# Performance work log

Hardware: AMD Instinct MI355X
Metric: run time of the kernel (lower is better)

The kernel has to match this reference:

```python
import jax, jax.numpy as jnp
import numpy as np

EMBED_DIM = 1024
NUM_HEADS = 16
HEAD_DIM = EMBED_DIM // NUM_HEADS
B, T = 4, 2048


def setup_inputs() -> dict:
    key = jax.random.key(0)
    ks = jax.random.split(key, 5)
    s = 1.0 / np.sqrt(EMBED_DIM)
    x = jax.random.normal(ks[0], (B, T, EMBED_DIM), dtype=jnp.float32)
    W_qkv = jax.random.uniform(ks[1], (EMBED_DIM, 3 * EMBED_DIM), minval=-s, maxval=s, dtype=jnp.float32)
    b_qkv = jax.random.uniform(ks[2], (3 * EMBED_DIM,), minval=-s, maxval=s, dtype=jnp.float32)
    W_proj = jax.random.uniform(ks[3], (EMBED_DIM, EMBED_DIM), minval=-s, maxval=s, dtype=jnp.float32)
    b_proj = jax.random.uniform(ks[4], (EMBED_DIM,), minval=-s, maxval=s, dtype=jnp.float32)
    return {"x": x, "W_qkv": W_qkv, "b_qkv": b_qkv, "W_proj": W_proj, "b_proj": b_proj}


def reference(x, W_qkv, b_qkv, W_proj, b_proj):
    Bq, Tq, C = x.shape
    H, D = NUM_HEADS, HEAD_DIM
    qkv = x @ W_qkv + b_qkv                      # [B,T,3C]
    qkv = qkv.reshape(Bq, Tq, 3, H, D)
    q = qkv[:, :, 0].transpose(0, 2, 1, 3)       # [B,H,T,D]
    k = qkv[:, :, 1].transpose(0, 2, 1, 3)
    v = qkv[:, :, 2].transpose(0, 2, 1, 3)
    scale = 1.0 / jnp.sqrt(jnp.asarray(D, x.dtype))
    attn = jnp.einsum('bhqd,bhkd->bhqk', q, k) * scale  # [B,H,T,T]
    mask = jnp.tril(jnp.ones((Tq, Tq), dtype=bool))     # causal: keep lower triangle
    attn = jnp.where(mask, attn, jnp.asarray(-jnp.inf, attn.dtype))
    attn = jax.nn.softmax(attn, axis=-1)
    out = jnp.einsum('bhqk,bhkd->bhqd', attn, v)        # [B,H,T,D]
    out = out.transpose(0, 2, 1, 3).reshape(Bq, Tq, C)
    return out @ W_proj + b_proj
```

## Files before the change

kernel.cpp:

```cpp
#include <hip/hip_runtime.h>
#include <stdint.h>

typedef unsigned short ushort_t;
typedef __attribute__((ext_vector_type(4))) unsigned int  u32x4;
typedef __attribute__((ext_vector_type(2))) unsigned int  u32x2;
typedef __attribute__((ext_vector_type(4))) float         f32x4;
typedef __attribute__((ext_vector_type(8))) __bf16        bf16x8;
typedef __attribute__((ext_vector_type(2))) __bf16        bf16x2;

__device__ __forceinline__ ushort_t f2bf(float f) {
    unsigned int u = __float_as_uint(f);
    u += 0x7fffu + ((u >> 16) & 1u);
    return (ushort_t)(u >> 16);
}
__device__ __forceinline__ unsigned int pack2bf(float a, float b) {
    return (unsigned int)f2bf(a) | ((unsigned int)f2bf(b) << 16);
}
#if __has_builtin(__builtin_amdgcn_cvt_pk_bf16_f32)
__device__ __forceinline__ unsigned int pack2bf_fast(float a, float b) {
    bf16x2 v = __builtin_amdgcn_cvt_pk_bf16_f32(a, b);
    return __builtin_bit_cast(unsigned int, v);
}
#else
__device__ __forceinline__ unsigned int pack2bf_fast(float a, float b) {
    return pack2bf(a, b);
}
#endif
__device__ __forceinline__ f32x4 mfma16(bf16x8 a, bf16x8 b, f32x4 c) {
    return __builtin_amdgcn_mfma_f32_16x16x32_bf16(a, b, c, 0, 0, 0);
}
__device__ __forceinline__ bf16x8 ldfrag(const ushort_t* p) {
    return __builtin_bit_cast(bf16x8, *(const u32x4*)p);
}

__device__ __forceinline__ void gld16(const ushort_t* g, ushort_t* l) {
    __builtin_amdgcn_global_load_lds(
        (const __attribute__((address_space(1))) void*)g,
        (__attribute__((address_space(3))) void*)l, 16, 0, 0);
}

__device__ __forceinline__ void wg_barrier() {
    asm volatile("s_waitcnt lgkmcnt(0)\n\ts_barrier" ::: "memory");
}

#define QSCALE 0.18033688011112042f

__global__ __launch_bounds__(256) void prep(const float* __restrict__ X,
                                            ushort_t* __restrict__ Xb,
                                            const float* __restrict__ Wq,
                                            ushort_t* __restrict__ Wqt,
                                            const float* __restrict__ Wp,
                                            ushort_t* __restrict__ Wpt) {
    __shared__ float tile[32][33];
    const int tid = threadIdx.x;
    const int b   = blockIdx.x;
    if (b < 4096) {
        long i = ((long)b * 256 + tid) * 8;
        float4 a = *(const float4*)(X + i);
        float4 c = *(const float4*)(X + i + 4);
        u32x4 pk;
        pk.x = pack2bf(a.x, a.y); pk.y = pack2bf(a.z, a.w);
        pk.z = pack2bf(c.x, c.y); pk.w = pack2bf(c.z, c.w);
        *(u32x4*)(Xb + i) = pk;
        return;
    }
    const float* W; ushort_t* Wt; int N, bx, by;
    if (b < 7168) { int idx = b - 4096; W = Wq; Wt = Wqt; N = 3072; bx = idx % 96; by = idx / 96; }
    else          { int idx = b - 7168; W = Wp; Wt = Wpt; N = 1024; bx = idx & 31; by = idx >> 5; }
    const int tx = tid & 31, ty = tid >> 5;
    const int n0 = bx * 32, k0 = by * 32;
    for (int p = 0; p < 4; ++p)
        tile[ty + 8*p][tx] = W[(long)(k0 + ty + 8*p) * N + n0 + tx];
    __syncthreads();
    for (int p = 0; p < 4; ++p)
        Wt[(long)(n0 + ty + 8*p) * 1024 + k0 + tx] = f2bf(tile[tx][ty + 8*p]);
}

__global__ __launch_bounds__(256) void gemm_qkv(const ushort_t* __restrict__ Xb,
                                                const ushort_t* __restrict__ Wt,
                                                const float* __restrict__ bias,
                                                ushort_t* __restrict__ Qo,
                                                ushort_t* __restrict__ Ko,
                                                ushort_t* __restrict__ Vto) {
    __shared__ __align__(16) ushort_t smem[24576];

    const int tid  = threadIdx.x;
    const int g    = blockIdx.x;
    const int grp  = g / 192, rr = g % 192;
    const int m0   = (grp * 8 + (rr & 7)) * 128;
    const int n0   = (rr >> 3) * 128;
    const int lane = tid & 63, w = tid >> 6;
    const int quad = lane >> 4, l16 = lane & 15;
    const int wm = (w >> 1) * 64, wn = (w & 1) * 64;

    const int srow  = tid >> 2;
    const int slot  = tid & 3;
    const int oct   = slot ^ ((tid >> 3) & 3);
    const int rslot = (quad ^ ((l16 >> 1) & 3)) * 8;
    const int wbase = (tid & 192) * 8;

    const ushort_t* Ap = Xb + (long)(m0 + srow) * 1024 + oct * 8;
    const ushort_t* Bp = Wt + (long)(n0 + srow) * 1024 + oct * 8;

    f32x4 acc[4][4] = {};

    auto issue = [&](int pf, int ibuf) {
        int k = (pf < 32) ? (pf << 5) : 0;
        gld16(Ap + k,         &smem[ibuf + wbase]);
        gld16(Ap + k + 65536, &smem[ibuf + wbase + 2048]);
        gld16(Bp + k,         &smem[ibuf + wbase + 4096]);
        gld16(Bp + k + 65536, &smem[ibuf + wbase + 6144]);
    };
    auto step = [&](int p, int rbuf, int ibuf) {
        asm volatile("s_waitcnt vmcnt(4)\n\ts_barrier" ::: "memory");
        issue(p + 2, ibuf);
        const ushort_t* As = smem + rbuf;
        const ushort_t* Bs = As + 4096;
        bf16x8 af[4], bfr[4];
        for (int i = 0; i < 4; ++i)
            af[i] = ldfrag(&As[(wm + 16*i + l16) * 32 + rslot]);
        for (int j = 0; j < 4; ++j)
            bfr[j] = ldfrag(&Bs[(wn + 16*j + l16) * 32 + rslot]);
        __builtin_amdgcn_s_setprio(1);
        for (int i = 0; i < 4; ++i)
            for (int j = 0; j < 4; ++j)
                acc[i][j] = mfma16(af[i], bfr[j], acc[i][j]);
        __builtin_amdgcn_s_setprio(0);
    };

    issue(0, 0);
    issue(1, 8192);
    for (int p = 0; p < 30; p += 3) {
        step(p,     0,     16384);
        step(p + 1, 8192,  0);
        step(p + 2, 16384, 8192);
    }
    step(30, 0,    16384);
    step(31, 8192, 0);

    float bj[4];
    for (int j = 0; j < 4; ++j) bj[j] = bias[n0 + wn + 16*j + l16];
    const int bb = m0 >> 11, t0m = m0 & 2047;
    asm volatile("s_waitcnt vmcnt(0)" ::: "memory");
    __syncthreads();

    if (n0 < 2048) {
        ushort_t* dst = (n0 < 1024) ? Qo : Ko;
        const float scale = (n0 < 1024) ? QSCALE : 1.0f;
        const int nbase = (n0 < 1024) ? n0 : n0 - 1024;
        for (int i = 0; i < 4; ++i)
            for (int j = 0; j < 4; ++j) {
                int nl = wn + 16*j + l16;
                for (int r = 0; r < 4; ++r) {
                    int ml = wm + 16*i + quad*4 + r;
                    smem[ml * 136 + nl] = f2bf((acc[i][j][r] + bj[j]) * scale);
                }
            }
        __syncthreads();
        for (int c = 0; c < 8; ++c) {
            int chunk = tid + 256 * c;
            int row = chunk >> 4, nc = (chunk & 15) * 8;
            int n = nbase + nc;
            int hh = n >> 6, d = n & 63;
            *(u32x4*)&dst[((long)(bb*16 + hh) * 2048 + t0m + row) * 64 + d] =
                *(const u32x4*)&smem[row * 136 + nc];
        }
    } else {
        for (int i = 0; i < 4; ++i)
            for (int j = 0; j < 4; ++j) {
                int nl = wn + 16*j + l16;
                for (int r = 0; r < 4; ++r) {
                    int ml = wm + 16*i + quad*4 + r;
                    smem[nl * 136 + ml] = f2bf(acc[i][j][r] + bj[j]);
                }
            }
        __syncthreads();
        for (int c = 0; c < 8; ++c) {
            int chunk = tid + 256 * c;
            int row = chunk >> 4, mc = (chunk & 15) * 8;
            int n = n0 - 2048 + row;
            int hh = n >> 6, d = n & 63;
            *(u32x4*)&Vto[((long)(bb*16 + hh) * 64 + d) * 2048 + t0m + mc] =
                *(const u32x4*)&smem[row * 136 + mc];
        }
    }
}

__global__ __launch_bounds__(256) void attn_kernel(const ushort_t* __restrict__ Q,
                                                   const ushort_t* __restrict__ K,
                                                   const ushort_t* __restrict__ Vt,
                                                   ushort_t* __restrict__ O) {
    __shared__ __align__(16) ushort_t Ks[2][64 * 64];
    __shared__ __align__(16) ushort_t Vs[2][64 * 64];
    __shared__ __align__(16) ushort_t Ps[128 * 72];

    const int tid  = threadIdx.x;
    const int lane = tid & 63, w = tid >> 6, quad = lane >> 4, l16 = lane & 15;
    const int g    = blockIdx.x;
    const int bh   = (g & 7) + 8 * ((g >> 3) & 7);
    const int qt   = 15 - (g >> 6);
    const ushort_t* qptr = Q  + (long)bh * 2048 * 64;
    const ushort_t* kptr = K  + (long)bh * 2048 * 64;
    const ushort_t* vptr = Vt + (long)bh * 64 * 2048;
    const int bb2 = bh >> 4, h = bh & 15;

    const int srow = tid >> 3;
    const int slot = tid & 7;
    const int oct  = slot ^ (srow & 7);
    const int koff = srow * 64 + oct * 8;
    const int voff = srow * 2048 + oct * 8;
    const int wofs = srow * 64 + slot * 8;

    const int qbase = qt * 128;
    const int nkt = 2 * qt + 2;

    for (int c = 0; c < 4; ++c) {
        int flat = tid + 256 * c;
        int row = flat >> 3, kc = (flat & 7) * 8;
        *(u32x4*)&Ps[row * 72 + kc] = *(const u32x4*)&qptr[(long)(qbase + row) * 64 + kc];
    }
    wg_barrier();
    bf16x8 qf[2][2];
    for (int nt = 0; nt < 2; ++nt)
        for (int kk = 0; kk < 2; ++kk)
            qf[nt][kk] = ldfrag(&Ps[(32*w + 16*nt + l16) * 72 + kk*32 + quad*8]);

    f32x4 acc[2][4] = {};
    float l_run[2] = {0.f, 0.f};

    auto phase = [&](int kt, ushort_t* Kb, ushort_t* Vb) {
        const int kbase = kt * 64;
        if (kbase > qbase + 32*w + 31) return;
        f32x4 s[4][2] = {};
        __builtin_amdgcn_s_setprio(1);
        for (int kk = 0; kk < 2; ++kk)
            for (int mt = 0; mt < 4; ++mt) {
                bf16x8 kf = ldfrag(&Kb[(16*mt + l16) * 64 + ((4*kk + quad) ^ (l16 & 7)) * 8]);
                for (int nt = 0; nt < 2; ++nt)
                    s[mt][nt] = mfma16(kf, qf[nt][kk], s[mt][nt]);
            }
        __builtin_amdgcn_s_setprio(0);
        if (kbase + 63 > qbase + 32*w) {
            for (int mt = 0; mt < 4; ++mt)
                for (int nt = 0; nt < 2; ++nt) {
                    int qv = qbase + 32*w + 16*nt + l16;
                    for (int r = 0; r < 4; ++r)
                        if (kbase + 16*mt + 4*quad + r > qv)
                            s[mt][nt][r] = -__builtin_inff();
                }
        }
        for (int nt = 0; nt < 2; ++nt)
            for (int mt = 0; mt < 4; ++mt) {
                float p0 = __builtin_amdgcn_exp2f(s[mt][nt][0]);
                float p1 = __builtin_amdgcn_exp2f(s[mt][nt][1]);
                float p2 = __builtin_amdgcn_exp2f(s[mt][nt][2]);
                float p3 = __builtin_amdgcn_exp2f(s[mt][nt][3]);
                l_run[nt] += (p0 + p1) + (p2 + p3);
                u32x2 pk;
                pk.x = pack2bf_fast(p0, p1);
                pk.y = pack2bf_fast(p2, p3);
                *(u32x2*)&Ps[(32*w + 16*nt + l16) * 72 + 16*mt + 4*quad] = pk;
            }
        __builtin_amdgcn_s_setprio(1);
        for (int kk = 0; kk < 2; ++kk) {
            bf16x8 pf0 = ldfrag(&Ps[(32*w + l16) * 72 + kk*32 + quad*8]);
            bf16x8 pf1 = ldfrag(&Ps[(32*w + 16 + l16) * 72 + kk*32 + quad*8]);
            for (int jd = 0; jd < 4; ++jd) {
                bf16x8 vf = ldfrag(&Vb[(16*jd + l16) * 64 + ((4*kk + quad) ^ (l16 & 7)) * 8]);
                acc[0][jd] = mfma16(pf0, vf, acc[0][jd]);
                acc[1][jd] = mfma16(pf1, vf, acc[1][jd]);
            }
        }
        __builtin_amdgcn_s_setprio(0);
    };

    u32x4 KA0 = *(const u32x4*)(kptr + koff);
    u32x4 KA1 = *(const u32x4*)(kptr + koff + 2048);
    u32x4 VA0 = *(const u32x4*)(vptr + voff);
    u32x4 VA1 = *(const u32x4*)(vptr + voff + 65536);
    u32x4 KB0 = *(const u32x4*)(kptr + 4096 + koff);
    u32x4 KB1 = *(const u32x4*)(kptr + 4096 + koff + 2048);
    u32x4 VB0 = *(const u32x4*)(vptr + 64 + voff);
    u32x4 VB1 = *(const u32x4*)(vptr + 64 + voff + 65536);

    for (int kt = 0; kt < nkt; kt += 2) {
        {
            *(u32x4*)&Ks[0][wofs]        = KA0;
            *(u32x4*)&Ks[0][wofs + 2048] = KA1;
            *(u32x4*)&Vs[0][wofs]        = VA0;
            *(u32x4*)&Vs[0][wofs + 2048] = VA1;
            int kf = (kt + 2 < nkt) ? kt + 2 : kt;
            KA0 = *(const u32x4*)(kptr + kf*4096 + koff);
            KA1 = *(const u32x4*)(kptr + kf*4096 + koff + 2048);
            VA0 = *(const u32x4*)(vptr + kf*64 + voff);
            VA1 = *(const u32x4*)(vptr + kf*64 + voff + 65536);
            wg_barrier();
            phase(kt, Ks[0], Vs[0]);
        }
        {
            *(u32x4*)&Ks[1][wofs]        = KB0;
            *(u32x4*)&Ks[1][wofs + 2048] = KB1;
            *(u32x4*)&Vs[1][wofs]        = VB0;
            *(u32x4*)&Vs[1][wofs + 2048] = VB1;
            int kf = (kt + 3 < nkt) ? kt + 3 : kt + 1;
            KB0 = *(const u32x4*)(kptr + kf*4096 + koff);
            KB1 = *(const u32x4*)(kptr + kf*4096 + koff + 2048);
            VB0 = *(const u32x4*)(vptr + kf*64 + voff);
            VB1 = *(const u32x4*)(vptr + kf*64 + voff + 65536);
            wg_barrier();
            phase(kt + 1, Ks[1], Vs[1]);
        }
    }

    for (int i = 0; i < 2; ++i) {
        float l = l_run[i];
        l += __shfl_xor(l, 16, 64);
        l += __shfl_xor(l, 32, 64);
        for (int r = 0; r < 4; ++r) {
            float linv = 1.0f / __shfl(l, (lane & 48) | (4*quad + r), 64);
            int t = qbase + 32*w + 16*i + 4*quad + r;
            for (int jd = 0; jd < 4; ++jd) {
                int d = 16*jd + l16;
                O[((long)(bb2*2048 + t)) * 1024 + h*64 + d] = f2bf(acc[i][jd][r] * linv);
            }
        }
    }
}

__global__ __launch_bounds__(256) void gemm_proj(const ushort_t* __restrict__ A,
                                                 const ushort_t* __restrict__ Wt,
                                                 const float* __restrict__ bias,
                                                 float* __restrict__ Out) {
    __shared__ __align__(16) ushort_t smem[24576];

    const int tid  = threadIdx.x;
    const int g    = blockIdx.x;
    const int grp  = g / 64, rr = g % 64;
    const int m0   = (grp * 8 + (rr & 7)) * 128;
    const int n0   = (rr >> 3) * 128;
    const int lane = tid & 63, w = tid >> 6;
    const int quad = lane >> 4, l16 = lane & 15;
    const int wm = (w >> 1) * 64, wn = (w & 1) * 64;

    const int srow  = tid >> 2;
    const int slot  = tid & 3;
    const int oct   = slot ^ ((tid >> 3) & 3);
    const int rslot = (quad ^ ((l16 >> 1) & 3)) * 8;
    const int wbase = (tid & 192) * 8;

    const ushort_t* Ap = A  + (long)(m0 + srow) * 1024 + oct * 8;
    const ushort_t* Bp = Wt + (long)(n0 + srow) * 1024 + oct * 8;

    f32x4 acc[4][4] = {};

    auto issue = [&](int pf, int ibuf) {
        int k = (pf < 32) ? (pf << 5) : 0;
        gld16(Ap + k,         &smem[ibuf + wbase]);
        gld16(Ap + k + 65536, &smem[ibuf + wbase + 2048]);
        gld16(Bp + k,         &smem[ibuf + wbase + 4096]);
        gld16(Bp + k + 65536, &smem[ibuf + wbase + 6144]);
    };
    auto step = [&](int p, int rbuf, int ibuf) {
        asm volatile("s_waitcnt vmcnt(4)\n\ts_barrier" ::: "memory");
        issue(p + 2, ibuf);
        const ushort_t* As = smem + rbuf;
        const ushort_t* Bs = As + 4096;
        bf16x8 af[4], bfr[4];
        for (int i = 0; i < 4; ++i)
            af[i] = ldfrag(&As[(wm + 16*i + l16) * 32 + rslot]);
        for (int j = 0; j < 4; ++j)
            bfr[j] = ldfrag(&Bs[(wn + 16*j + l16) * 32 + rslot]);
        __builtin_amdgcn_s_setprio(1);
        for (int i = 0; i < 4; ++i)
            for (int j = 0; j < 4; ++j)
                acc[i][j] = mfma16(af[i], bfr[j], acc[i][j]);
        __builtin_amdgcn_s_setprio(0);
    };

    issue(0, 0);
    issue(1, 8192);
    for (int p = 0; p < 30; p += 3) {
        step(p,     0,     16384);
        step(p + 1, 8192,  0);
        step(p + 2, 16384, 8192);
    }
    step(30, 0,    16384);
    step(31, 8192, 0);
    asm volatile("s_waitcnt vmcnt(0)" ::: "memory");

    float bj[4];
    for (int j = 0; j < 4; ++j) bj[j] = bias[n0 + wn + 16*j + l16];
    for (int i = 0; i < 4; ++i)
        for (int j = 0; j < 4; ++j)
            for (int r = 0; r < 4; ++r) {
                int m = m0 + wm + 16*i + quad*4 + r;
                int n = n0 + wn + 16*j + l16;
                Out[(long)m * 1024 + n] = acc[i][j][r] + bj[j];
            }
}

extern "C" void kernel_launch(void* const* d_in, const int* in_sizes, int n_in,
                              void* d_out, int out_size, void* d_ws, size_t ws_size,
                              hipStream_t stream) {
    const float* x     = (const float*)d_in[0];
    const float* Wqkv  = (const float*)d_in[1];
    const float* bqkv  = (const float*)d_in[2];
    const float* Wproj = (const float*)d_in[3];
    const float* bproj = (const float*)d_in[4];
    float* out = (float*)d_out;

    ushort_t* wqkvt  = (ushort_t*)d_ws;
    ushort_t* wprojt = wqkvt  + 3072 * 1024;
    ushort_t* Qb     = wprojt + 1024 * 1024;
    ushort_t* Kb     = Qb  + 8388608;
    ushort_t* Vtb    = Kb  + 8388608;
    ushort_t* XbA2   = Vtb + 8388608;

    prep<<<8192, 256, 0, stream>>>(x, XbA2, Wqkv, wqkvt, Wproj, wprojt);
    gemm_qkv<<<1536, 256, 0, stream>>>(XbA2, wqkvt, bqkv, Qb, Kb, Vtb);
    attn_kernel<<<1024, 256, 0, stream>>>(Qb, Kb, Vtb, XbA2);
    gemm_proj<<<512, 256, 0, stream>>>(XbA2, wprojt, bproj, out);
}
```

Before: 242.4 us.

## Load GEMM A fragments directly from global into registers, keep only B in LDS

Both the QKV and projection GEMMs stop staging the activation (A) tile through shared memory. Each wave now loads its own A MFMA fragments straight from global memory into registers, one k-step ahead. Only the weight tile still uses the global-to-LDS triple buffer, which shrinks LDS use and raises the launch-bounds occupancy hint to 3 blocks. The cost is redundant global A loads, since waves sharing rows each fetch them, plus more exposed global-load latency because the register prefetch is only one step deep.

```diff
diff --git a/kernel.cpp b/kernel.cpp
--- a/kernel.cpp
+++ b/kernel.cpp
@@ -31,6 +31,9 @@
 }
 __device__ __forceinline__ bf16x8 ldfrag(const ushort_t* p) {
     return __builtin_bit_cast(bf16x8, *(const u32x4*)p);
+}
+__device__ __forceinline__ bf16x8 asfrag(u32x4 v) {
+    return __builtin_bit_cast(bf16x8, v);
 }
 
 __device__ __forceinline__ void gld16(const ushort_t* g, ushort_t* l) {
@@ -76,13 +79,13 @@
         Wt[(long)(n0 + ty + 8*p) * 1024 + k0 + tx] = f2bf(tile[tx][ty + 8*p]);
 }
 
-__global__ __launch_bounds__(256) void gemm_qkv(const ushort_t* __restrict__ Xb,
-                                                const ushort_t* __restrict__ Wt,
-                                                const float* __restrict__ bias,
-                                                ushort_t* __restrict__ Qo,
-                                                ushort_t* __restrict__ Ko,
-                                                ushort_t* __restrict__ Vto) {
-    __shared__ __align__(16) ushort_t smem[24576];
+__global__ __launch_bounds__(256, 3) void gemm_qkv(const ushort_t* __restrict__ Xb,
+                                                   const ushort_t* __restrict__ Wt,
+                                                   const float* __restrict__ bias,
+                                                   ushort_t* __restrict__ Qo,
+                                                   ushort_t* __restrict__ Ko,
+                                                   ushort_t* __restrict__ Vto) {
+    __shared__ __align__(16) ushort_t smem[17408];
 
     const int tid  = threadIdx.x;
     const int g    = blockIdx.x;
@@ -99,44 +102,45 @@
     const int rslot = (quad ^ ((l16 >> 1) & 3)) * 8;
     const int wbase = (tid & 192) * 8;
 
-    const ushort_t* Ap = Xb + (long)(m0 + srow) * 1024 + oct * 8;
     const ushort_t* Bp = Wt + (long)(n0 + srow) * 1024 + oct * 8;
+    const ushort_t* A0 = Xb + (long)(m0 + wm + l16) * 1024 + quad * 8;
 
     f32x4 acc[4][4] = {};
-
-    auto issue = [&](int pf, int ibuf) {
+    u32x4 acur[4];
+
+    auto issueB = [&](int pf, int ibuf) {
         int k = (pf < 32) ? (pf << 5) : 0;
-        gld16(Ap + k,         &smem[ibuf + wbase]);
-        gld16(Ap + k + 65536, &smem[ibuf + wbase + 2048]);
-        gld16(Bp + k,         &smem[ibuf + wbase + 4096]);
-        gld16(Bp + k + 65536, &smem[ibuf + wbase + 6144]);
+        gld16(Bp + k,         &smem[ibuf + wbase]);
+        gld16(Bp + k + 65536, &smem[ibuf + wbase + 2048]);
     };
     auto step = [&](int p, int rbuf, int ibuf) {
-        asm volatile("s_waitcnt vmcnt(4)\n\ts_barrier" ::: "memory");
-        issue(p + 2, ibuf);
-        const ushort_t* As = smem + rbuf;
-        const ushort_t* Bs = As + 4096;
-        bf16x8 af[4], bfr[4];
-        for (int i = 0; i < 4; ++i)
-            af[i] = ldfrag(&As[(wm + 16*i + l16) * 32 + rslot]);
+        asm volatile("s_waitcnt vmcnt(6)\n\ts_barrier" ::: "memory");
+        issueB(p + 2, ibuf);
+        const ushort_t* Bs = smem + rbuf;
+        bf16x8 bfr[4];
         for (int j = 0; j < 4; ++j)
             bfr[j] = ldfrag(&Bs[(wn + 16*j + l16) * 32 + rslot]);
         __builtin_amdgcn_s_setprio(1);
         for (int i = 0; i < 4; ++i)
             for (int j = 0; j < 4; ++j)
-                acc[i][j] = mfma16(af[i], bfr[j], acc[i][j]);
+                acc[i][j] = mfma16(asfrag(acur[i]), bfr[j], acc[i][j]);
         __builtin_amdgcn_s_setprio(0);
+        int kn = (p + 1 < 32) ? ((p + 1) << 5) : 0;
+        for (int i = 0; i < 4; ++i)
+            acur[i] = *(const u32x4*)(A0 + i * 16384 + kn);
     };
 
-    issue(0, 0);
-    issue(1, 8192);
+    issueB(0, 0);
+    issueB(1, 4096);
+    for (int i = 0; i < 4; ++i)
+        acur[i] = *(const u32x4*)(A0 + i * 16384);
     for (int p = 0; p < 30; p += 3) {
-        step(p,     0,     16384);
-        step(p + 1, 8192,  0);
-        step(p + 2, 16384, 8192);
-    }
-    step(30, 0,    16384);
-    step(31, 8192, 0);
+        step(p,     0,    8192);
+        step(p + 1, 4096, 0);
+        step(p + 2, 8192, 4096);
+    }
+    step(30, 0,    8192);
+    step(31, 4096, 0);
 
     float bj[4];
     for (int j = 0; j < 4; ++j) bj[j] = bias[n0 + wn + 16*j + l16];
@@ -327,11 +331,11 @@
     }
 }
 
-__global__ __launch_bounds__(256) void gemm_proj(const ushort_t* __restrict__ A,
-                                                 const ushort_t* __restrict__ Wt,
-                                                 const float* __restrict__ bias,
-                                                 float* __restrict__ Out) {
-    __shared__ __align__(16) ushort_t smem[24576];
+__global__ __launch_bounds__(256, 3) void gemm_proj(const ushort_t* __restrict__ A,
+                                                    const ushort_t* __restrict__ Wt,
+                                                    const float* __restrict__ bias,
+                                                    float* __restrict__ Out) {
+    __shared__ __align__(16) ushort_t smem[12288];
 
     const int tid  = threadIdx.x;
     const int g    = blockIdx.x;
@@ -348,44 +352,45 @@
     const int rslot = (quad ^ ((l16 >> 1) & 3)) * 8;
     const int wbase = (tid & 192) * 8;
 
-    const ushort_t* Ap = A  + (long)(m0 + srow) * 1024 + oct * 8;
     const ushort_t* Bp = Wt + (long)(n0 + srow) * 1024 + oct * 8;
+    const ushort_t* A0 = A + (long)(m0 + wm + l16) * 1024 + quad * 8;
 
     f32x4 acc[4][4] = {};
-
-    auto issue = [&](int pf, int ibuf) {
+    u32x4 acur[4];
+
+    auto issueB = [&](int pf, int ibuf) {
         int k = (pf < 32) ? (pf << 5) : 0;
-        gld16(Ap + k,         &smem[ibuf + wbase]);
-        gld16(Ap + k + 65536, &smem[ibuf + wbase + 2048]);
-        gld16(Bp + k,         &smem[ibuf + wbase + 4096]);
-        gld16(Bp + k + 65536, &smem[ibuf + wbase + 6144]);
+        gld16(Bp + k,         &smem[ibuf + wbase]);
+        gld16(Bp + k + 65536, &smem[ibuf + wbase + 2048]);
     };
     auto step = [&](int p, int rbuf, int ibuf) {
-        asm volatile("s_waitcnt vmcnt(4)\n\ts_barrier" ::: "memory");
-        issue(p + 2, ibuf);
-        const ushort_t* As = smem + rbuf;
-        const ushort_t* Bs = As + 4096;
-        bf16x8 af[4], bfr[4];
-        for (int i = 0; i < 4; ++i)
-            af[i] = ldfrag(&As[(wm + 16*i + l16) * 32 + rslot]);
+        asm volatile("s_waitcnt vmcnt(6)\n\ts_barrier" ::: "memory");
+        issueB(p + 2, ibuf);
+        const ushort_t* Bs = smem + rbuf;
+        bf16x8 bfr[4];
         for (int j = 0; j < 4; ++j)
             bfr[j] = ldfrag(&Bs[(wn + 16*j + l16) * 32 + rslot]);
         __builtin_amdgcn_s_setprio(1);
         for (int i = 0; i < 4; ++i)
             for (int j = 0; j < 4; ++j)
-                acc[i][j] = mfma16(af[i], bfr[j], acc[i][j]);
+                acc[i][j] = mfma16(asfrag(acur[i]), bfr[j], acc[i][j]);
         __builtin_amdgcn_s_setprio(0);
+        int kn = (p + 1 < 32) ? ((p + 1) << 5) : 0;
+        for (int i = 0; i < 4; ++i)
+            acur[i] = *(const u32x4*)(A0 + i * 16384 + kn);
     };
 
-    issue(0, 0);
-    issue(1, 8192);
+    issueB(0, 0);
+    issueB(1, 4096);
+    for (int i = 0; i < 4; ++i)
+        acur[i] = *(const u32x4*)(A0 + i * 16384);
     for (int p = 0; p < 30; p += 3) {
-        step(p,     0,     16384);
-        step(p + 1, 8192,  0);
-        step(p + 2, 16384, 8192);
-    }
-    step(30, 0,    16384);
-    step(31, 8192, 0);
+        step(p,     0,    8192);
+        step(p + 1, 4096, 0);
+        step(p + 2, 8192, 4096);
+    }
+    step(30, 0,    8192);
+    step(31, 4096, 0);
     asm volatile("s_waitcnt vmcnt(0)" ::: "memory");
 
     float bj[4];
```

After: 302.6 us. +24.9%, slower.

## Enlarge QKV GEMM tiles to 256x256 with 512-thread blocks

Applied to the files above, without the earlier changes.

The QKV projection GEMM moves from 128x128 tiles with 256 threads to 256x256 tiles with 512 threads (8 waves, each computing 128x64). It uses a double-buffered pipeline with split MFMA phases and a new XCD-aware block swizzle. The epilogue is staged through LDS in four passes to fit the larger tile. The aim is more operand reuse per global load and fewer blocks, at the cost of extra barriers and register pressure. With 384 blocks the grid may not fill all CUs evenly.

```diff
diff --git a/kernel.cpp b/kernel.cpp
--- a/kernel.cpp
+++ b/kernel.cpp
@@ -76,17 +76,288 @@
         Wt[(long)(n0 + ty + 8*p) * 1024 + k0 + tx] = f2bf(tile[tx][ty + 8*p]);
 }
 
-__global__ __launch_bounds__(256) void gemm_qkv(const ushort_t* __restrict__ Xb,
-                                                const ushort_t* __restrict__ Wt,
-                                                const float* __restrict__ bias,
-                                                ushort_t* __restrict__ Qo,
-                                                ushort_t* __restrict__ Ko,
-                                                ushort_t* __restrict__ Vto) {
-    __shared__ __align__(16) ushort_t smem[24576];
+__global__ __launch_bounds__(512, 4) void gemm_qkv(const ushort_t* __restrict__ Xb,
+                                                   const ushort_t* __restrict__ Wt,
+                                                   const float* __restrict__ bias,
+                                                   ushort_t* __restrict__ Qo,
+                                                   ushort_t* __restrict__ Ko,
+                                                   ushort_t* __restrict__ Vto) {
+    __shared__ __align__(16) ushort_t smem[32768];
 
     const int tid  = threadIdx.x;
     const int g    = blockIdx.x;
-    const int grp  = g / 192, rr = g % 192;
+    const int swz  = (g & 7) * 48 + (g >> 3);
+    const int m0   = (swz & 31) * 256;
+    const int n0   = (swz >> 5) * 256;
+    const int lane = tid & 63, w = tid >> 6;
+    const int quad = lane >> 4, l16 = lane & 15;
+    const int wm   = (w >> 2) * 128, wn = (w & 3) * 64;
+
+    const int srow  = tid >> 2;
+    const int slot  = tid & 3;
+    const int oct   = slot ^ ((tid >> 3) & 3);
+    const int rslot = (quad ^ ((l16 >> 1) & 3)) * 8;
+
+    const ushort_t* ApL = Xb + (long)(m0 + srow) * 1024 + oct * 8;
+    const ushort_t* ApH = ApL + 131072;
+    const ushort_t* BpL = Wt + (long)(n0 + srow) * 1024 + oct * 8;
+    const ushort_t* BpH = BpL + 131072;
+
+    f32x4 acc[8][4] = {};
+
+    auto issue_tile = [&](int kt, int bbase) {
+        int k = (kt < 32) ? (kt << 5) : 0;
+        gld16(ApL + k, &smem[bbase + tid * 8]);
+        gld16(ApH + k, &smem[bbase + 4096 + tid * 8]);
+        gld16(BpL + k, &smem[bbase + 8192 + tid * 8]);
+        gld16(BpH + k, &smem[bbase + 12288 + tid * 8]);
+    };
+
+    auto tile_step = [&](int t, int rb, int ib) {
+        const ushort_t* As = smem + rb;
+        const ushort_t* Bs = smem + rb + 8192;
+        bf16x8 af[4], bfj[4];
+        for (int i = 0; i < 4; ++i)
+            af[i] = ldfrag(&As[(wm + 16*i + l16) * 32 + rslot]);
+        for (int j = 0; j < 4; ++j)
+            bfj[j] = ldfrag(&Bs[(wn + 16*j + l16) * 32 + rslot]);
+        issue_tile(t + 1, ib);
+        asm volatile("s_barrier" ::: "memory");
+        __builtin_amdgcn_sched_barrier(0);
+        __builtin_amdgcn_s_setprio(1);
+        for (int i = 0; i < 4; ++i)
+            for (int j = 0; j < 4; ++j)
+                acc[i][j] = mfma16(af[i], bfj[j], acc[i][j]);
+        __builtin_amdgcn_s_setprio(0);
+        asm volatile("s_barrier" ::: "memory");
+        bf16x8 ag[4];
+        for (int i = 0; i < 4; ++i)
+            ag[i] = ldfrag(&As[(wm + 64 + 16*i + l16) * 32 + rslot]);
+        asm volatile("s_barrier" ::: "memory");
+        __builtin_amdgcn_sched_barrier(0);
+        __builtin_amdgcn_s_setprio(1);
+        for (int i = 0; i < 4; ++i)
+            for (int j = 0; j < 4; ++j)
+                acc[4 + i][j] = mfma16(ag[i], bfj[j], acc[4 + i][j]);
+        __builtin_amdgcn_s_setprio(0);
+        asm volatile("s_waitcnt vmcnt(0)\n\ts_barrier" ::: "memory");
+    };
+
+    issue_tile(0, 0);
+    asm volatile("s_waitcnt vmcnt(0)\n\ts_barrier" ::: "memory");
+    for (int t = 0; t < 32; t += 2) {
+        tile_step(t,     0,     16384);
+        tile_step(t + 1, 16384, 0);
+    }
+
+    float bj[4];
+    for (int j = 0; j < 4; ++j) bj[j] = bias[n0 + wn + 16*j + l16];
+    const int bb = m0 >> 11, t0m = m0 & 2047;
+    __syncthreads();
+
+    if (n0 < 2048) {
+        ushort_t* dst = (n0 < 1024) ? Qo : Ko;
+        const float scale = (n0 < 1024) ? QSCALE : 1.0f;
+        const int nbase = (n0 < 1024) ? n0 : n0 - 1024;
+        for (int p = 0; p < 4; ++p) {
+            if (wm == (p >> 1) * 128) {
+                int i0 = (p & 1) * 4;
+                for (int ii = 0; ii < 4; ++ii)
+                    for (int j = 0; j < 4; ++j) {
+                        int nl = wn + 16*j + l16;
+                        for (int r = 0; r < 4; ++r) {
+                            int lr = 16*ii + quad*4 + r;
+                            smem[lr * 264 + nl] = f2bf((acc[i0 + ii][j][r] + bj[j]) * scale);
+                        }
+                    }
+            }
+            __syncthreads();
+            for (int c = 0; c < 4; ++c) {
+                int chunk = tid + 512 * c;
+                int row = chunk >> 5, nc = (chunk & 31) * 8;
+                int n = nbase + nc;
+                int hh = n >> 6, d = n & 63;
+                *(u32x4*)&dst[((long)(bb*16 + hh) * 2048 + t0m + 64*p + row) * 64 + d] =
+                    *(const u32x4*)&smem[row * 264 + nc];
+            }
+            __syncthreads();
+        }
+    } else {
+        for (int p = 0; p < 4; ++p) {
+            if (wn == 64 * p) {
+                for (int i = 0; i < 8; ++i)
+                    for (int j = 0; j < 4; ++j) {
+                        int nl = 16*j + l16;
+                        for (int r = 0; r < 4; ++r) {
+                            int ml = wm + 16*i + quad*4 + r;
+                            smem[nl * 264 + ml] = f2bf(acc[i][j][r] + bj[j]);
+                        }
+                    }
+            }
+            __syncthreads();
+            for (int c = 0; c < 4; ++c) {
+                int chunk = tid + 512 * c;
+                int nr = chunk >> 5, mc = (chunk & 31) * 8;
+                int n = n0 - 2048 + 64*p + nr;
+                int hh = n >> 6, d = n & 63;
+                *(u32x4*)&Vto[((long)(bb*16 + hh) * 64 + d) * 2048 + t0m + mc] =
+                    *(const u32x4*)&smem[nr * 264 + mc];
+            }
+            __syncthreads();
+        }
+    }
+}
+
+__global__ __launch_bounds__(256) void attn_kernel(const ushort_t* __restrict__ Q,
+                                                   const ushort_t* __restrict__ K,
+                                                   const ushort_t* __restrict__ Vt,
+                                                   ushort_t* __restrict__ O) {
+    __shared__ __align__(16) ushort_t Ks[2][64 * 64];
+    __shared__ __align__(16) ushort_t Vs[2][64 * 64];
+    __shared__ __align__(16) ushort_t Ps[128 * 72];
+
+    const int tid  = threadIdx.x;
+    const int lane = tid & 63, w = tid >> 6, quad = lane >> 4, l16 = lane & 15;
+    const int g    = blockIdx.x;
+    const int bh   = (g & 7) + 8 * ((g >> 3) & 7);
+    const int qt   = 15 - (g >> 6);
+    const ushort_t* qptr = Q  + (long)bh * 2048 * 64;
+    const ushort_t* kptr = K  + (long)bh * 2048 * 64;
+    const ushort_t* vptr = Vt + (long)bh * 64 * 2048;
+    const int bb2 = bh >> 4, h = bh & 15;
+
+    const int srow = tid >> 3;
+    const int slot = tid & 7;
+    const int oct  = slot ^ (srow & 7);
+    const int koff = srow * 64 + oct * 8;
+    const int voff = srow * 2048 + oct * 8;
+    const int wofs = srow * 64 + slot * 8;
+
+    const int qbase = qt * 128;
+    const int nkt = 2 * qt + 2;
+
+    for (int c = 0; c < 4; ++c) {
+        int flat = tid + 256 * c;
+        int row = flat >> 3, kc = (flat & 7) * 8;
+        *(u32x4*)&Ps[row * 72 + kc] = *(const u32x4*)&qptr[(long)(qbase + row) * 64 + kc];
+    }
+    wg_barrier();
+    bf16x8 qf[2][2];
+    for (int nt = 0; nt < 2; ++nt)
+        for (int kk = 0; kk < 2; ++kk)
+            qf[nt][kk] = ldfrag(&Ps[(32*w + 16*nt + l16) * 72 + kk*32 + quad*8]);
+
+    f32x4 acc[2][4] = {};
+    float l_run[2] = {0.f, 0.f};
+
+    auto phase = [&](int kt, ushort_t* Kb, ushort_t* Vb) {
+        const int kbase = kt * 64;
+        if (kbase > qbase + 32*w + 31) return;
+        f32x4 s[4][2] = {};
+        __builtin_amdgcn_s_setprio(1);
+        for (int kk = 0; kk < 2; ++kk)
+            for (int mt = 0; mt < 4; ++mt) {
+                bf16x8 kf = ldfrag(&Kb[(16*mt + l16) * 64 + ((4*kk + quad) ^ (l16 & 7)) * 8]);
+                for (int nt = 0; nt < 2; ++nt)
+                    s[mt][nt] = mfma16(kf, qf[nt][kk], s[mt][nt]);
+            }
+        __builtin_amdgcn_s_setprio(0);
+        if (kbase + 63 > qbase + 32*w) {
+            for (int mt = 0; mt < 4; ++mt)
+                for (int nt = 0; nt < 2; ++nt) {
+                    int qv = qbase + 32*w + 16*nt + l16;
+                    for (int r = 0; r < 4; ++r)
+                        if (kbase + 16*mt + 4*quad + r > qv)
+                            s[mt][nt][r] = -__builtin_inff();
+                }
+        }
+        for (int nt = 0; nt < 2; ++nt)
+            for (int mt = 0; mt < 4; ++mt) {
+                float p0 = __builtin_amdgcn_exp2f(s[mt][nt][0]);
+                float p1 = __builtin_amdgcn_exp2f(s[mt][nt][1]);
+                float p2 = __builtin_amdgcn_exp2f(s[mt][nt][2]);
+                float p3 = __builtin_amdgcn_exp2f(s[mt][nt][3]);
+                l_run[nt] += (p0 + p1) + (p2 + p3);
+                u32x2 pk;
+                pk.x = pack2bf_fast(p0, p1);
+                pk.y = pack2bf_fast(p2, p3);
+                *(u32x2*)&Ps[(32*w + 16*nt + l16) * 72 + 16*mt + 4*quad] = pk;
+            }
+        __builtin_amdgcn_s_setprio(1);
+        for (int kk = 0; kk < 2; ++kk) {
+            bf16x8 pf0 = ldfrag(&Ps[(32*w + l16) * 72 + kk*32 + quad*8]);
+            bf16x8 pf1 = ldfrag(&Ps[(32*w + 16 + l16) * 72 + kk*32 + quad*8]);
+            for (int jd = 0; jd < 4; ++jd) {
+                bf16x8 vf = ldfrag(&Vb[(16*jd + l16) * 64 + ((4*kk + quad) ^ (l16 & 7)) * 8]);
+                acc[0][jd] = mfma16(pf0, vf, acc[0][jd]);
+                acc[1][jd] = mfma16(pf1, vf, acc[1][jd]);
+            }
+        }
+        __builtin_amdgcn_s_setprio(0);
+    };
+
+    u32x4 KA0 = *(const u32x4*)(kptr + koff);
+    u32x4 KA1 = *(const u32x4*)(kptr + koff + 2048);
+    u32x4 VA0 = *(const u32x4*)(vptr + voff);
+    u32x4 VA1 = *(const u32x4*)(vptr + voff + 65536);
+    u32x4 KB0 = *(const u32x4*)(kptr + 4096 + koff);
+    u32x4 KB1 = *(const u32x4*)(kptr + 4096 + koff + 2048);
+    u32x4 VB0 = *(const u32x4*)(vptr + 64 + voff);
+    u32x4 VB1 = *(const u32x4*)(vptr + 64 + voff + 65536);
+
+    for (int kt = 0; kt < nkt; kt += 2) {
+        {
+            *(u32x4*)&Ks[0][wofs]        = KA0;
+            *(u32x4*)&Ks[0][wofs + 2048] = KA1;
+            *(u32x4*)&Vs[0][wofs]        = VA0;
+            *(u32x4*)&Vs[0][wofs + 2048] = VA1;
+            int kf = (kt + 2 < nkt) ? kt + 2 : kt;
+            KA0 = *(const u32x4*)(kptr + kf*4096 + koff);
+            KA1 = *(const u32x4*)(kptr + kf*4096 + koff + 2048);
+            VA0 = *(const u32x4*)(vptr + kf*64 + voff);
+            VA1 = *(const u32x4*)(vptr + kf*64 + voff + 65536);
+            wg_barrier();
+            phase(kt, Ks[0], Vs[0]);
+        }
+        {
+            *(u32x4*)&Ks[1][wofs]        = KB0;
+            *(u32x4*)&Ks[1][wofs + 2048] = KB1;
+            *(u32x4*)&Vs[1][wofs]        = VB0;
+            *(u32x4*)&Vs[1][wofs + 2048] = VB1;
+            int kf = (kt + 3 < nkt) ? kt + 3 : kt + 1;
+            KB0 = *(const u32x4*)(kptr + kf*4096 + koff);
+            KB1 = *(const u32x4*)(kptr + kf*4096 + koff + 2048);
+            VB0 = *(const u32x4*)(vptr + kf*64 + voff);
+            VB1 = *(const u32x4*)(vptr + kf*64 + voff + 65536);
+            wg_barrier();
+            phase(kt + 1, Ks[1], Vs[1]);
+        }
+    }
+
+    for (int i = 0; i < 2; ++i) {
+        float l = l_run[i];
+        l += __shfl_xor(l, 16, 64);
+        l += __shfl_xor(l, 32, 64);
+        for (int r = 0; r < 4; ++r) {
+            float linv = 1.0f / __shfl(l, (lane & 48) | (4*quad + r), 64);
+            int t = qbase + 32*w + 16*i + 4*quad + r;
+            for (int jd = 0; jd < 4; ++jd) {
+                int d = 16*jd + l16;
+                O[((long)(bb2*2048 + t)) * 1024 + h*64 + d] = f2bf(acc[i][jd][r] * linv);
+            }
+        }
+    }
+}
+
+__global__ __launch_bounds__(256) void gemm_proj(const ushort_t* __restrict__ A,
+                                                 const ushort_t* __restrict__ Wt,
+                                                 const float* __restrict__ bias,
+                                                 float* __restrict__ Out) {
+    __shared__ __align__(16) ushort_t smem[24576];
+
+    const int tid  = threadIdx.x;
+    const int g    = blockIdx.x;
+    const int grp  = g / 64, rr = g % 64;
     const int m0   = (grp * 8 + (rr & 7)) * 128;
     const int n0   = (rr >> 3) * 128;
     const int lane = tid & 63, w = tid >> 6;
@@ -99,7 +370,7 @@
     const int rslot = (quad ^ ((l16 >> 1) & 3)) * 8;
     const int wbase = (tid & 192) * 8;
 
-    const ushort_t* Ap = Xb + (long)(m0 + srow) * 1024 + oct * 8;
+    const ushort_t* Ap = A  + (long)(m0 + srow) * 1024 + oct * 8;
     const ushort_t* Bp = Wt + (long)(n0 + srow) * 1024 + oct * 8;
 
     f32x4 acc[4][4] = {};
@@ -137,255 +408,6 @@
     }
     step(30, 0,    16384);
     step(31, 8192, 0);
-
-    float bj[4];
-    for (int j = 0; j < 4; ++j) bj[j] = bias[n0 + wn + 16*j + l16];
-    const int bb = m0 >> 11, t0m = m0 & 2047;
-    asm volatile("s_waitcnt vmcnt(0)" ::: "memory");
-    __syncthreads();
-
-    if (n0 < 2048) {
-        ushort_t* dst = (n0 < 1024) ? Qo : Ko;
-        const float scale = (n0 < 1024) ? QSCALE : 1.0f;
-        const int nbase = (n0 < 1024) ? n0 : n0 - 1024;
-        for (int i = 0; i < 4; ++i)
-            for (int j = 0; j < 4; ++j) {
-                int nl = wn + 16*j + l16;
-                for (int r = 0; r < 4; ++r) {
-                    int ml = wm + 16*i + quad*4 + r;
-                    smem[ml * 136 + nl] = f2bf((acc[i][j][r] + bj[j]) * scale);
-                }
-            }
-        __syncthreads();
-        for (int c = 0; c < 8; ++c) {
-            int chunk = tid + 256 * c;
-            int row = chunk >> 4, nc = (chunk & 15) * 8;
-            int n = nbase + nc;
-            int hh = n >> 6, d = n & 63;
-            *(u32x4*)&dst[((long)(bb*16 + hh) * 2048 + t0m + row) * 64 + d] =
-                *(const u32x4*)&smem[row * 136 + nc];
-        }
-    } else {
-        for (int i = 0; i < 4; ++i)
-            for (int j = 0; j < 4; ++j) {
-                int nl = wn + 16*j + l16;
-                for (int r = 0; r < 4; ++r) {
-                    int ml = wm + 16*i + quad*4 + r;
-                    smem[nl * 136 + ml] = f2bf(acc[i][j][r] + bj[j]);
-                }
-            }
-        __syncthreads();
-        for (int c = 0; c < 8; ++c) {
-            int chunk = tid + 256 * c;
-            int row = chunk >> 4, mc = (chunk & 15) * 8;
-            int n = n0 - 2048 + row;
-            int hh = n >> 6, d = n & 63;
-            *(u32x4*)&Vto[((long)(bb*16 + hh) * 64 + d) * 2048 + t0m + mc] =
-                *(const u32x4*)&smem[row * 136 + mc];
-        }
-    }
-}
-
-__global__ __launch_bounds__(256) void attn_kernel(const ushort_t* __restrict__ Q,
-                                                   const ushort_t* __restrict__ K,
-                                                   const ushort_t* __restrict__ Vt,
-                                                   ushort_t* __restrict__ O) {
-    __shared__ __align__(16) ushort_t Ks[2][64 * 64];
-    __shared__ __align__(16) ushort_t Vs[2][64 * 64];
-    __shared__ __align__(16) ushort_t Ps[128 * 72];
-
-    const int tid  = threadIdx.x;
-    const int lane = tid & 63, w = tid >> 6, quad = lane >> 4, l16 = lane & 15;
-    const int g    = blockIdx.x;
-    const int bh   = (g & 7) + 8 * ((g >> 3) & 7);
-    const int qt   = 15 - (g >> 6);
-    const ushort_t* qptr = Q  + (long)bh * 2048 * 64;
-    const ushort_t* kptr = K  + (long)bh * 2048 * 64;
-    const ushort_t* vptr = Vt + (long)bh * 64 * 2048;
-    const int bb2 = bh >> 4, h = bh & 15;
-
-    const int srow = tid >> 3;
-    const int slot = tid & 7;
-    const int oct  = slot ^ (srow & 7);
-    const int koff = srow * 64 + oct * 8;
-    const int voff = srow * 2048 + oct * 8;
-    const int wofs = srow * 64 + slot * 8;
-
-    const int qbase = qt * 128;
-    const int nkt = 2 * qt + 2;
-
-    for (int c = 0; c < 4; ++c) {
-        int flat = tid + 256 * c;
-        int row = flat >> 3, kc = (flat & 7) * 8;
-        *(u32x4*)&Ps[row * 72 + kc] = *(const u32x4*)&qptr[(long)(qbase + row) * 64 + kc];
-    }
-    wg_barrier();
-    bf16x8 qf[2][2];
-    for (int nt = 0; nt < 2; ++nt)
-        for (int kk = 0; kk < 2; ++kk)
-            qf[nt][kk] = ldfrag(&Ps[(32*w + 16*nt + l16) * 72 + kk*32 + quad*8]);
-
-    f32x4 acc[2][4] = {};
-    float l_run[2] = {0.f, 0.f};
-
-    auto phase = [&](int kt, ushort_t* Kb, ushort_t* Vb) {
-        const int kbase = kt * 64;
-        if (kbase > qbase + 32*w + 31) return;
-        f32x4 s[4][2] = {};
-        __builtin_amdgcn_s_setprio(1);
-        for (int kk = 0; kk < 2; ++kk)
-            for (int mt = 0; mt < 4; ++mt) {
-                bf16x8 kf = ldfrag(&Kb[(16*mt + l16) * 64 + ((4*kk + quad) ^ (l16 & 7)) * 8]);
-                for (int nt = 0; nt < 2; ++nt)
-                    s[mt][nt] = mfma16(kf, qf[nt][kk], s[mt][nt]);
-            }
-        __builtin_amdgcn_s_setprio(0);
-        if (kbase + 63 > qbase + 32*w) {
-            for (int mt = 0; mt < 4; ++mt)
-                for (int nt = 0; nt < 2; ++nt) {
-                    int qv = qbase + 32*w + 16*nt + l16;
-                    for (int r = 0; r < 4; ++r)
-                        if (kbase + 16*mt + 4*quad + r > qv)
-                            s[mt][nt][r] = -__builtin_inff();
-                }
-        }
-        for (int nt = 0; nt < 2; ++nt)
-            for (int mt = 0; mt < 4; ++mt) {
-                float p0 = __builtin_amdgcn_exp2f(s[mt][nt][0]);
-                float p1 = __builtin_amdgcn_exp2f(s[mt][nt][1]);
-                float p2 = __builtin_amdgcn_exp2f(s[mt][nt][2]);
-                float p3 = __builtin_amdgcn_exp2f(s[mt][nt][3]);
-                l_run[nt] += (p0 + p1) + (p2 + p3);
-                u32x2 pk;
-                pk.x = pack2bf_fast(p0, p1);
-                pk.y = pack2bf_fast(p2, p3);
-                *(u32x2*)&Ps[(32*w + 16*nt + l16) * 72 + 16*mt + 4*quad] = pk;
-            }
-        __builtin_amdgcn_s_setprio(1);
-        for (int kk = 0; kk < 2; ++kk) {
-            bf16x8 pf0 = ldfrag(&Ps[(32*w + l16) * 72 + kk*32 + quad*8]);
-            bf16x8 pf1 = ldfrag(&Ps[(32*w + 16 + l16) * 72 + kk*32 + quad*8]);
-            for (int jd = 0; jd < 4; ++jd) {
-                bf16x8 vf = ldfrag(&Vb[(16*jd + l16) * 64 + ((4*kk + quad) ^ (l16 & 7)) * 8]);
-                acc[0][jd] = mfma16(pf0, vf, acc[0][jd]);
-                acc[1][jd] = mfma16(pf1, vf, acc[1][jd]);
-            }
-        }
-        __builtin_amdgcn_s_setprio(0);
-    };
-
-    u32x4 KA0 = *(const u32x4*)(kptr + koff);
-    u32x4 KA1 = *(const u32x4*)(kptr + koff + 2048);
-    u32x4 VA0 = *(const u32x4*)(vptr + voff);
-    u32x4 VA1 = *(const u32x4*)(vptr + voff + 65536);
-    u32x4 KB0 = *(const u32x4*)(kptr + 4096 + koff);
-    u32x4 KB1 = *(const u32x4*)(kptr + 4096 + koff + 2048);
-    u32x4 VB0 = *(const u32x4*)(vptr + 64 + voff);
-    u32x4 VB1 = *(const u32x4*)(vptr + 64 + voff + 65536);
-
-    for (int kt = 0; kt < nkt; kt += 2) {
-        {
-            *(u32x4*)&Ks[0][wofs]        = KA0;
-            *(u32x4*)&Ks[0][wofs + 2048] = KA1;
-            *(u32x4*)&Vs[0][wofs]        = VA0;
-            *(u32x4*)&Vs[0][wofs + 2048] = VA1;
-            int kf = (kt + 2 < nkt) ? kt + 2 : kt;
-            KA0 = *(const u32x4*)(kptr + kf*4096 + koff);
-            KA1 = *(const u32x4*)(kptr + kf*4096 + koff + 2048);
-            VA0 = *(const u32x4*)(vptr + kf*64 + voff);
-            VA1 = *(const u32x4*)(vptr + kf*64 + voff + 65536);
-            wg_barrier();
-            phase(kt, Ks[0], Vs[0]);
-        }
-        {
-            *(u32x4*)&Ks[1][wofs]        = KB0;
-            *(u32x4*)&Ks[1][wofs + 2048] = KB1;
-            *(u32x4*)&Vs[1][wofs]        = VB0;
-            *(u32x4*)&Vs[1][wofs + 2048] = VB1;
-            int kf = (kt + 3 < nkt) ? kt + 3 : kt + 1;
-            KB0 = *(const u32x4*)(kptr + kf*4096 + koff);
-            KB1 = *(const u32x4*)(kptr + kf*4096 + koff + 2048);
-            VB0 = *(const u32x4*)(vptr + kf*64 + voff);
-            VB1 = *(const u32x4*)(vptr + kf*64 + voff + 65536);
-            wg_barrier();
-            phase(kt + 1, Ks[1], Vs[1]);
-        }
-    }
-
-    for (int i = 0; i < 2; ++i) {
-        float l = l_run[i];
-        l += __shfl_xor(l, 16, 64);
-        l += __shfl_xor(l, 32, 64);
-        for (int r = 0; r < 4; ++r) {
-            float linv = 1.0f / __shfl(l, (lane & 48) | (4*quad + r), 64);
-            int t = qbase + 32*w + 16*i + 4*quad + r;
-            for (int jd = 0; jd < 4; ++jd) {
-                int d = 16*jd + l16;
-                O[((long)(bb2*2048 + t)) * 1024 + h*64 + d] = f2bf(acc[i][jd][r] * linv);
-            }
-        }
-    }
-}
-
-__global__ __launch_bounds__(256) void gemm_proj(const ushort_t* __restrict__ A,
-                                                 const ushort_t* __restrict__ Wt,
-                                                 const float* __restrict__ bias,
-                                                 float* __restrict__ Out) {
-    __shared__ __align__(16) ushort_t smem[24576];
-
-    const int tid  = threadIdx.x;
-    const int g    = blockIdx.x;
-    const int grp  = g / 64, rr = g % 64;
-    const int m0   = (grp * 8 + (rr & 7)) * 128;
-    const int n0   = (rr >> 3) * 128;
-    const int lane = tid & 63, w = tid >> 6;
-    const int quad = lane >> 4, l16 = lane & 15;
-    const int wm = (w >> 1) * 64, wn = (w & 1) * 64;
-
-    const int srow  = tid >> 2;
-    const int slot  = tid & 3;
-    const int oct   = slot ^ ((tid >> 3) & 3);
-    const int rslot = (quad ^ ((l16 >> 1) & 3)) * 8;
-    const int wbase = (tid & 192) * 8;
-
-    const ushort_t* Ap = A  + (long)(m0 + srow) * 1024 + oct * 8;
-    const ushort_t* Bp = Wt + (long)(n0 + srow) * 1024 + oct * 8;
-
-    f32x4 acc[4][4] = {};
-
-    auto issue = [&](int pf, int ibuf) {
-        int k = (pf < 32) ? (pf << 5) : 0;
-        gld16(Ap + k,         &smem[ibuf + wbase]);
-        gld16(Ap + k + 65536, &smem[ibuf + wbase + 2048]);
-        gld16(Bp + k,         &smem[ibuf + wbase + 4096]);
-        gld16(Bp + k + 65536, &smem[ibuf + wbase + 6144]);
-    };
-    auto step = [&](int p, int rbuf, int ibuf) {
-        asm volatile("s_waitcnt vmcnt(4)\n\ts_barrier" ::: "memory");
-        issue(p + 2, ibuf);
-        const ushort_t* As = smem + rbuf;
-        const ushort_t* Bs = As + 4096;
-        bf16x8 af[4], bfr[4];
-        for (int i = 0; i < 4; ++i)
-            af[i] = ldfrag(&As[(wm + 16*i + l16) * 32 + rslot]);
-        for (int j = 0; j < 4; ++j)
-            bfr[j] = ldfrag(&Bs[(wn + 16*j + l16) * 32 + rslot]);
-        __builtin_amdgcn_s_setprio(1);
-        for (int i = 0; i < 4; ++i)
-            for (int j = 0; j < 4; ++j)
-                acc[i][j] = mfma16(af[i], bfr[j], acc[i][j]);
-        __builtin_amdgcn_s_setprio(0);
-    };
-
-    issue(0, 0);
-    issue(1, 8192);
-    for (int p = 0; p < 30; p += 3) {
-        step(p,     0,     16384);
-        step(p + 1, 8192,  0);
-        step(p + 2, 16384, 8192);
-    }
-    step(30, 0,    16384);
-    step(31, 8192, 0);
     asm volatile("s_waitcnt vmcnt(0)" ::: "memory");
 
     float bj[4];
@@ -417,7 +439,7 @@
     ushort_t* XbA2   = Vtb + 8388608;
 
     prep<<<8192, 256, 0, stream>>>(x, XbA2, Wqkv, wqkvt, Wproj, wprojt);
-    gemm_qkv<<<1536, 256, 0, stream>>>(XbA2, wqkvt, bqkv, Qb, Kb, Vtb);
+    gemm_qkv<<<384, 512, 0, stream>>>(XbA2, wqkvt, bqkv, Qb, Kb, Vtb);
     attn_kernel<<<1024, 256, 0, stream>>>(Qb, Kb, Vtb, XbA2);
     gemm_proj<<<512, 256, 0, stream>>>(XbA2, wprojt, bproj, out);
 }
```

Measured after the change: 771.9 us. +218.5%, slower.
